# Optimization experiments

Measured on AMD Instinct MI355X. Metric: run time of the kernel, lower is better.

## Reference

```python
import jax, jax.numpy as jnp
import numpy as np

B, S, D = 4, 512, 2048      # batch, seq, hidden
DFF = 5632                   # SwiGLU intermediate
E, TOPK, R = 8, 2, 16        # experts, top-k, lora rank
SCALE = 32.0 / 16.0          # lora alpha / r


def setup_inputs() -> dict:
    key = jax.random.key(0)
    ks = jax.random.split(key, 18)
    rn = lambda k, shape, s=0.02: (jax.random.normal(k, shape, dtype=jnp.float32) * s)
    return {
        "data": jax.random.normal(ks[0], (B, S, D), dtype=jnp.float32),
        # shared base SwiGLU MLP (gate/up/down projections)
        "W1": rn(ks[1], (DFF, D)),
        "W3": rn(ks[2], (DFF, D)),
        "W2": rn(ks[3], (D, DFF)),
        # MixLoRA MoE adapter: router gate + per-expert LoRA on w1/w3/w2
        "gate_W": rn(ks[4], (E, D)),
        "A1": rn(ks[5], (E, R, D)), "B1": rn(ks[6], (E, DFF, R)),
        "A3": rn(ks[7], (E, R, D)), "B3": rn(ks[8], (E, DFF, R)),
        "A2": rn(ks[9], (E, R, DFF)), "B2": rn(ks[10], (E, D, R)),
        # plain LoRA adapter (second batch segment, _lora_forward path)
        "la1": rn(ks[11], (R, D)), "lb1": rn(ks[12], (DFF, R)),
        "la3": rn(ks[13], (R, D)), "lb3": rn(ks[14], (DFF, R)),
        "la2": rn(ks[15], (R, DFF)), "lb2": rn(ks[16], (D, R)),
    }


def reference(data, W1, W3, W2, gate_W, A1, B1, A3, B3, A2, B2,
              la1, lb1, la3, lb3, la2, lb2):
    half = B // 2

    # ---- segment 0: MixLoRA MoE adapter ----
    x = data[:half].reshape(-1, D)                      # [N, D] tokens
    N = x.shape[0]
    logits = x @ gate_W.T                               # [N, E] router logits
    probs = jax.nn.softmax(logits, axis=-1)
    topw, topi = jax.lax.top_k(probs, TOPK)
    topw = topw / jnp.sum(topw, axis=-1, keepdims=True)
    # dense routing weights (zero for non-selected experts)
    wd = jnp.zeros((N, E), x.dtype).at[jnp.arange(N)[:, None], topi].set(topw)

    bg = x @ W1.T                                       # [N, DFF] base gate proj
    bu = x @ W3.T                                       # [N, DFF] base up proj
    dg = jnp.einsum('enr,efr->enf', jnp.einsum('nd,erd->enr', x, A1), B1)
    du = jnp.einsum('enr,efr->enf', jnp.einsum('nd,erd->enr', x, A3), B3)
    h = jax.nn.silu(bg[None] + SCALE * dg) * (bu[None] + SCALE * du)  # [E,N,DFF]
    oe = jnp.einsum('enf,df->end', h, W2) \
        + SCALE * jnp.einsum('enr,edr->end', jnp.einsum('enf,erf->enr', h, A2), B2)
    moe_out = jnp.einsum('ne,end->nd', wd, oe).reshape(half, S, D)

    # ---- segment 1: plain LoRA adapter (_lora_forward) ----
    x2 = data[half:]                                    # [half, S, D]
    g2 = jax.nn.silu(x2 @ W1.T + SCALE * ((x2 @ la1.T) @ lb1.T))
    u2 = x2 @ W3.T + SCALE * ((x2 @ la3.T) @ lb3.T)
    h2 = g2 * u2
    out2 = h2 @ W2.T + SCALE * ((h2 @ la2.T) @ lb2.T)

    # index_copy over contiguous per-segment ranges == concat along dim 0
    final = jnp.concatenate([moe_out, out2], axis=0)    # [B, S, D]
    return final, logits
```

## Files before the change

### kernel.cpp

```cpp
#include <hip/hip_runtime.h>
#include <hip/hip_bf16.h>

#define DEVI __device__ __forceinline__

typedef __attribute__((ext_vector_type(8))) short short8;
typedef __attribute__((ext_vector_type(4))) float f32x4;

constexpr int D    = 2048;
constexpr int DFF  = 5632;
constexpr int NTOK = 2048;
constexpr int NMOE = 1024;
constexpr float KSCALE = 2.0f;

constexpr int NW      = 11776;
constexpr int COL_A1  = 11264;
constexpr int COL_A3  = 11392;
constexpr int COL_LA1 = 11520;
constexpr int COL_LA3 = 11536;

DEVI float bf2f(unsigned short u) { return __uint_as_float(((unsigned)u) << 16); }
DEVI unsigned short f2bf(float f) {
  unsigned u = __float_as_uint(f);
  u += 0x7FFFu + ((u >> 16) & 1u);
  return (unsigned short)(u >> 16);
}
DEVI float silu(float x) { return x / (1.f + __expf(-x)); }

struct CastSegs {
  const float* src[14];
  unsigned short* dst[14];
  int blk_end[14];
};

__global__ __launch_bounds__(256) void cast_segs_kernel(CastSegs cs) {
  int b = blockIdx.x;
  int s = 0;
  #pragma unroll
  for (int i = 0; i < 14; ++i) if (b >= cs.blk_end[i]) s = i + 1;
  int bstart = (s == 0) ? 0 : cs.blk_end[s - 1];
  size_t idx = ((size_t)(b - bstart) * 256 + threadIdx.x) * 4;
  float4 v = *(const float4*)(cs.src[s] + idx);
  ushort4 o;
  o.x = f2bf(v.x); o.y = f2bf(v.y); o.z = f2bf(v.z); o.w = f2bf(v.w);
  *(ushort4*)(cs.dst[s] + idx) = o;
}

__global__ __launch_bounds__(256) void transpose_ra_kernel(const float* __restrict__ A2,
                                                           const float* __restrict__ la2,
                                                           unsigned short* __restrict__ A2tb,
                                                           unsigned short* __restrict__ la2tb) {
  int f = blockIdx.x * 256 + threadIdx.x;
  int e = blockIdx.y;
  const float* src = (e < 8) ? (A2 + (size_t)e * 16 * DFF) : la2;
  unsigned short* dst = (e < 8) ? (A2tb + (size_t)e * DFF * 16) : la2tb;
  unsigned short tmp[16];
  #pragma unroll
  for (int r = 0; r < 16; ++r) tmp[r] = f2bf(src[(size_t)r * DFF + f]);
  #pragma unroll
  for (int r = 0; r < 16; ++r) dst[(size_t)f * 16 + r] = tmp[r];
}

__global__ __launch_bounds__(256) void gate_kernel(const float* __restrict__ x,
                                                   const float* __restrict__ gW,
                                                   float* __restrict__ logits_out,
                                                   int* __restrict__ gidx,
                                                   float* __restrict__ gwt) {
  int t = blockIdx.x * 4 + (threadIdx.x >> 6);
  int lane = threadIdx.x & 63;
  const float* xr = x + (size_t)t * D;
  float acc[8];
  #pragma unroll
  for (int e = 0; e < 8; ++e) acc[e] = 0.f;
  for (int k = lane; k < D; k += 64) {
    float xv = xr[k];
    #pragma unroll
    for (int e = 0; e < 8; ++e) acc[e] = fmaf(xv, gW[e * D + k], acc[e]);
  }
  #pragma unroll
  for (int e = 0; e < 8; ++e) {
    float v = acc[e];
    #pragma unroll
    for (int s = 32; s > 0; s >>= 1) v += __shfl_xor(v, s);
    acc[e] = v;
  }
  if (lane == 0) {
    #pragma unroll
    for (int e = 0; e < 8; ++e) logits_out[(size_t)t * 8 + e] = acc[e];
    int i1 = 0;
    #pragma unroll
    for (int e = 1; e < 8; ++e) if (acc[e] > acc[i1]) i1 = e;
    int i2 = (i1 == 0) ? 1 : 0;
    #pragma unroll
    for (int e = 0; e < 8; ++e) if (e != i1 && acc[e] > acc[i2]) i2 = e;
    float w1 = 1.f / (1.f + expf(acc[i2] - acc[i1]));
    gidx[t * 2] = i1; gidx[t * 2 + 1] = i2;
    gwt[t * 2] = w1;  gwt[t * 2 + 1] = 1.f - w1;
  }
}

typedef const void __attribute__((address_space(1)))* gp1_t;
typedef void __attribute__((address_space(3)))* lp3_t;
DEVI void gload_lds16(const void* g, void* l) {
  __builtin_amdgcn_global_load_lds((gp1_t)g, (lp3_t)l, 16, 0, 0);
}
#define S_BARRIER() asm volatile("s_barrier" ::: "memory")

template <int N> DEVI void vmcnt_() {
  static_assert(N == 0 || N == 4 || N == 6 || N == 8 || N == 12, "enumerate literals");
  if constexpr (N == 0)  asm volatile("s_waitcnt vmcnt(0)" ::: "memory");
  if constexpr (N == 4)  asm volatile("s_waitcnt vmcnt(4)" ::: "memory");
  if constexpr (N == 6)  asm volatile("s_waitcnt vmcnt(6)" ::: "memory");
  if constexpr (N == 8)  asm volatile("s_waitcnt vmcnt(8)" ::: "memory");
  if constexpr (N == 12) asm volatile("s_waitcnt vmcnt(12)" ::: "memory");
}

template <int BM, int BN, int WM, int WN, int NBUF, int NPH, int MINW, int EPI>
__global__ __launch_bounds__(WM * WN * 64, MINW) void gemmT(
    const unsigned short* __restrict__ A,
    const unsigned short* __restrict__ B,
    int K,
    float* __restrict__ Cf,
    unsigned short* __restrict__ Cb,
    const float* __restrict__ addv,
    int ldc, int nbx) {
  constexpr int THREADS = WM * WN * 64;
  constexpr int RW = BM / WM;
  constexpr int CW = BN / WN;
  constexpr int FM = RW / 16, FN = CW / 16;
  constexpr int FMP = FM / NPH;
  constexpr int ATILE = BM * 128;
  constexpr int BTILE = BN * 128;
  constexpr int SLOT = ATILE + BTILE;
  constexpr int APARTS = BM * 8 / THREADS;
  constexpr int BPARTS = BN * 8 / THREADS;
  constexpr int LOADS = APARTS + BPARTS;
  constexpr int PD = NBUF - 1;

  __shared__ __align__(16) char smem[NBUF * SLOT];

  const int tid = threadIdx.x;
  const int wave = tid >> 6, lane = tid & 63;
  const int wm = wave / WN, wn = wave % WN;
  const int r15 = lane & 15, g = lane >> 4;

  const int nwg = (int)gridDim.x;
  const int bid = (int)blockIdx.x;
  const int wgid = (bid & 7) * (nwg >> 3) + (bid >> 3);
  const int bx = wgid % nbx, by = wgid / nbx;

  const unsigned short* Ablk = A + (size_t)by * BM * K;
  const unsigned short* Bblk = B + (size_t)bx * BN * K;

  int sgoA[APARTS], sgoB[BPARTS];
  #pragma unroll
  for (int j = 0; j < APARTS; ++j) {
    int tt = j * THREADS + tid;
    int row = tt >> 3;
    sgoA[j] = row * K + (((tt & 7) ^ (row & 7)) << 3);
  }
  #pragma unroll
  for (int j = 0; j < BPARTS; ++j) {
    int tt = j * THREADS + tid;
    int row = tt >> 3;
    sgoB[j] = row * K + (((tt & 7) ^ (row & 7)) << 3);
  }
  auto stage = [&](int slot, int k0) {
    char* s = smem + slot * SLOT;
    #pragma unroll
    for (int j = 0; j < APARTS; ++j)
      gload_lds16((const char*)Ablk + ((size_t)(sgoA[j] + k0) << 1),
                  s + j * (THREADS * 16) + wave * 1024);
    #pragma unroll
    for (int j = 0; j < BPARTS; ++j)
      gload_lds16((const char*)Bblk + ((size_t)(sgoB[j] + k0) << 1),
                  s + ATILE + j * (THREADS * 16) + wave * 1024);
  };

  const int arow0 = (wm * RW + r15) * 128;
  const int brow0 = (wn * CW + r15) * 128;
  const int s0 = ((g ^ (r15 & 7)) << 4);
  const int s1 = (((4 + g) ^ (r15 & 7)) << 4);

  f32x4 acc[FM][FN];
  #pragma unroll
  for (int m = 0; m < FM; ++m)
    #pragma unroll
    for (int n = 0; n < FN; ++n)
      #pragma unroll
      for (int j = 0; j < 4; ++j) acc[m][n][j] = 0.f;

  const int NT = K >> 6;

  #pragma unroll
  for (int d = 0; d < PD; ++d) stage(d, d << 6);

  int slCur = 0, slAhead = PD % NBUF;
  for (int t = 0; t < NT; ++t) {
    if (t + PD < NT) {
      stage(slAhead, (t + PD) << 6);
      vmcnt_<PD * LOADS>();
    } else if (PD == 2 && t + 1 < NT) {
      vmcnt_<LOADS>();
    } else {
      vmcnt_<0>();
    }
    S_BARRIER();

    const char* sA = smem + slCur * SLOT;
    const char* sB = sA + ATILE;
    short8 bq[FN][2];
    #pragma unroll
    for (int n = 0; n < FN; ++n) {
      bq[n][0] = *(const short8*)(sB + brow0 + n * 16 * 128 + s0);
      bq[n][1] = *(const short8*)(sB + brow0 + n * 16 * 128 + s1);
    }
    #pragma unroll
    for (int p = 0; p < NPH; ++p) {
      short8 af[FMP][2];
      #pragma unroll
      for (int i = 0; i < FMP; ++i) {
        int ro = arow0 + (p * FMP + i) * 16 * 128;
        af[i][0] = *(const short8*)(sA + ro + s0);
        af[i][1] = *(const short8*)(sA + ro + s1);
      }
      __builtin_amdgcn_s_setprio(1);
      #pragma unroll
      for (int i = 0; i < FMP; ++i)
        #pragma unroll
        for (int n = 0; n < FN; ++n)
          #pragma unroll
          for (int kk = 0; kk < 2; ++kk)
            acc[p * FMP + i][n] = __builtin_amdgcn_mfma_f32_16x16x32_bf16(
                af[i][kk], bq[n][kk], acc[p * FMP + i][n], 0, 0, 0);
      __builtin_amdgcn_s_setprio(0);
    }
    S_BARRIER();
    slCur = (slCur + 1 == NBUF) ? 0 : slCur + 1;
    slAhead = (slAhead + 1 == NBUF) ? 0 : slAhead + 1;
  }

  const int row0 = by * BM + wm * RW + (g << 2);
  const int col0 = bx * BN + wn * CW + r15;
  #pragma unroll
  for (int m = 0; m < FM; ++m) {
    #pragma unroll
    for (int n = 0; n < FN; ++n) {
      int col = col0 + n * 16;
      #pragma unroll
      for (int j = 0; j < 4; ++j) {
        int row = row0 + m * 16 + j;
        size_t off = (size_t)row * ldc + col;
        float v = acc[m][n][j];
        if (EPI == 1) Cb[off] = f2bf(v);
        else          Cf[off] = v + addv[off];
      }
    }
  }
}

DEVI float dot16bf(const float* a, const unsigned short* w) {
  short8 w0 = *(const short8*)w;
  short8 w1 = *(const short8*)(w + 8);
  float s = 0.f;
  #pragma unroll
  for (int i = 0; i < 8; ++i) s = fmaf(a[i],     bf2f((unsigned short)w0[i]), s);
  #pragma unroll
  for (int i = 0; i < 8; ++i) s = fmaf(a[8 + i], bf2f((unsigned short)w1[i]), s);
  return s;
}

__global__ __launch_bounds__(256) void h_kernel(
    const unsigned short* __restrict__ GU,
    const unsigned short* __restrict__ B1b,
    const unsigned short* __restrict__ B3b,
    const unsigned short* __restrict__ A2tb,
    const unsigned short* __restrict__ lb1b,
    const unsigned short* __restrict__ lb3b,
    const unsigned short* __restrict__ la2tb,
    const int* __restrict__ gidx, const float* __restrict__ gwt,
    unsigned short* __restrict__ Hb,
    float* __restrict__ qw) {
  const int t = blockIdx.x;
  const int tid = threadIdx.x;
  const unsigned short* gu = GU + (size_t)t * NW;
  unsigned short* hrow = Hb + (size_t)t * DFF;
  float qacc[32];
  #pragma unroll
  for (int r = 0; r < 32; ++r) qacc[r] = 0.f;
  float w1 = 0.f, w2 = 0.f;

  if (t < NMOE) {
    const int e1 = gidx[t * 2], e2 = gidx[t * 2 + 1];
    w1 = gwt[t * 2]; w2 = gwt[t * 2 + 1];
    float xa1a[16], xa1b[16], xa3a[16], xa3b[16];
    #pragma unroll
    for (int r = 0; r < 16; ++r) {
      xa1a[r] = bf2f(gu[COL_A1 + e1 * 16 + r]);
      xa1b[r] = bf2f(gu[COL_A1 + e2 * 16 + r]);
      xa3a[r] = bf2f(gu[COL_A3 + e1 * 16 + r]);
      xa3b[r] = bf2f(gu[COL_A3 + e2 * 16 + r]);
    }
    const unsigned short* B1e1 = B1b + (size_t)e1 * DFF * 16;
    const unsigned short* B1e2 = B1b + (size_t)e2 * DFF * 16;
    const unsigned short* B3e1 = B3b + (size_t)e1 * DFF * 16;
    const unsigned short* B3e2 = B3b + (size_t)e2 * DFF * 16;
    const unsigned short* A2e1 = A2tb + (size_t)e1 * DFF * 16;
    const unsigned short* A2e2 = A2tb + (size_t)e2 * DFF * 16;
    for (int i = 0; i < 22; ++i) {
      int f = tid + i * 256;
      float bg = bf2f(gu[f]), bu = bf2f(gu[DFF + f]);
      float dg1 = dot16bf(xa1a, B1e1 + f * 16);
      float du1 = dot16bf(xa3a, B3e1 + f * 16);
      float dg2 = dot16bf(xa1b, B1e2 + f * 16);
      float du2 = dot16bf(xa3b, B3e2 + f * 16);
      float h1 = silu(bg + KSCALE * dg1) * (bu + KSCALE * du1);
      float h2 = silu(bg + KSCALE * dg2) * (bu + KSCALE * du2);
      hrow[f] = f2bf(w1 * h1 + w2 * h2);
      short8 a0 = *(const short8*)(A2e1 + f * 16);
      short8 a1 = *(const short8*)(A2e1 + f * 16 + 8);
      short8 b0 = *(const short8*)(A2e2 + f * 16);
      short8 b1 = *(const short8*)(A2e2 + f * 16 + 8);
      #pragma unroll
      for (int r = 0; r < 8; ++r) {
        qacc[r]      = fmaf(h1, bf2f((unsigned short)a0[r]), qacc[r]);
        qacc[8 + r]  = fmaf(h1, bf2f((unsigned short)a1[r]), qacc[8 + r]);
        qacc[16 + r] = fmaf(h2, bf2f((unsigned short)b0[r]), qacc[16 + r]);
        qacc[24 + r] = fmaf(h2, bf2f((unsigned short)b1[r]), qacc[24 + r]);
      }
    }
  } else {
    float s1[16], s3[16];
    #pragma unroll
    for (int r = 0; r < 16; ++r) {
      s1[r] = bf2f(gu[COL_LA1 + r]);
      s3[r] = bf2f(gu[COL_LA3 + r]);
    }
    for (int i = 0; i < 22; ++i) {
      int f = tid + i * 256;
      float bg = bf2f(gu[f]), bu = bf2f(gu[DFF + f]);
      float dg = dot16bf(s1, lb1b + f * 16);
      float du = dot16bf(s3, lb3b + f * 16);
      float h = silu(bg + KSCALE * dg) * (bu + KSCALE * du);
      hrow[f] = f2bf(h);
      short8 a0 = *(const short8*)(la2tb + f * 16);
      short8 a1 = *(const short8*)(la2tb + f * 16 + 8);
      #pragma unroll
      for (int r = 0; r < 8; ++r) {
        qacc[r]     = fmaf(h, bf2f((unsigned short)a0[r]), qacc[r]);
        qacc[8 + r] = fmaf(h, bf2f((unsigned short)a1[r]), qacc[8 + r]);
      }
    }
  }

  #pragma unroll
  for (int r = 0; r < 32; ++r) {
    float v = qacc[r];
    #pragma unroll
    for (int s = 32; s > 0; s >>= 1) v += __shfl_xor(v, s);
    qacc[r] = v;
  }
  __shared__ float red[4][32];
  const int wave = tid >> 6, lane = tid & 63;
  if (lane == 0) {
    #pragma unroll
    for (int r = 0; r < 32; ++r) red[wave][r] = qacc[r];
  }
  __syncthreads();
  if (tid < 32) {
    float v = red[0][tid] + red[1][tid] + red[2][tid] + red[3][tid];
    float sc = (t < NMOE) ? ((tid < 16) ? (KSCALE * w1) : (KSCALE * w2)) : KSCALE;
    qw[(size_t)t * 32 + tid] = v * sc;
  }
}

__global__ __launch_bounds__(256) void ylora_kernel(const float* __restrict__ qw,
                                                    const unsigned short* __restrict__ B2b,
                                                    const unsigned short* __restrict__ lb2b,
                                                    const int* __restrict__ gidx,
                                                    float* __restrict__ ylora) {
  const int t = blockIdx.x;
  const int tid = threadIdx.x;
  const float* qr = qw + (size_t)t * 32;
  float q1[16], q2[16];
  #pragma unroll
  for (int r = 0; r < 16; ++r) { q1[r] = qr[r]; q2[r] = qr[16 + r]; }
  if (t < NMOE) {
    const unsigned short* p1 = B2b + (size_t)gidx[t * 2] * D * 16;
    const unsigned short* p2 = B2b + (size_t)gidx[t * 2 + 1] * D * 16;
    #pragma unroll
    for (int i = 0; i < 8; ++i) {
      int d = tid + i * 256;
      ylora[(size_t)t * D + d] = dot16bf(q1, p1 + d * 16) + dot16bf(q2, p2 + d * 16);
    }
  } else {
    #pragma unroll
    for (int i = 0; i < 8; ++i) {
      int d = tid + i * 256;
      ylora[(size_t)t * D + d] = dot16bf(q1, lb2b + d * 16);
    }
  }
}

extern "C" void kernel_launch(void* const* d_in, const int* in_sizes, int n_in,
                              void* d_out, int out_size, void* d_ws, size_t ws_size,
                              hipStream_t stream) {
  (void)in_sizes; (void)n_in; (void)out_size; (void)ws_size;
  const float* data = (const float*)d_in[0];
  const float* W1   = (const float*)d_in[1];
  const float* W3   = (const float*)d_in[2];
  const float* W2   = (const float*)d_in[3];
  const float* gW   = (const float*)d_in[4];
  const float* A1   = (const float*)d_in[5];
  const float* B1   = (const float*)d_in[6];
  const float* A3   = (const float*)d_in[7];
  const float* B3   = (const float*)d_in[8];
  const float* A2   = (const float*)d_in[9];
  const float* B2   = (const float*)d_in[10];
  const float* la1  = (const float*)d_in[11];
  const float* lb1  = (const float*)d_in[12];
  const float* la3  = (const float*)d_in[13];
  const float* lb3  = (const float*)d_in[14];
  const float* la2  = (const float*)d_in[15];
  const float* lb2  = (const float*)d_in[16];

  char* w = (char*)d_ws;
  size_t off = 0;
  auto alloc = [&](size_t bytes) -> char* {
    char* p = w + off;
    off += (bytes + 255) & ~(size_t)255;
    return p;
  };
  unsigned short* xb    = (unsigned short*)alloc((size_t)NTOK * D * 2);
  unsigned short* W13b  = (unsigned short*)alloc((size_t)NW * D * 2);
  unsigned short* W2b   = (unsigned short*)alloc((size_t)D * DFF * 2);
  unsigned short* B1b   = (unsigned short*)alloc((size_t)8 * DFF * 16 * 2);
  unsigned short* B3b   = (unsigned short*)alloc((size_t)8 * DFF * 16 * 2);
  unsigned short* A2tb  = (unsigned short*)alloc((size_t)8 * DFF * 16 * 2);
  unsigned short* la2tb = (unsigned short*)alloc((size_t)DFF * 16 * 2);
  unsigned short* lb1b  = (unsigned short*)alloc((size_t)DFF * 16 * 2);
  unsigned short* lb3b  = (unsigned short*)alloc((size_t)DFF * 16 * 2);
  unsigned short* lb2b  = (unsigned short*)alloc((size_t)D * 16 * 2);
  unsigned short* B2b   = (unsigned short*)alloc((size_t)8 * D * 16 * 2);
  int*   gidx = (int*)alloc((size_t)NMOE * 2 * 4);
  float* gwt  = (float*)alloc((size_t)NMOE * 2 * 4);
  unsigned short* GU    = (unsigned short*)alloc((size_t)NTOK * NW * 2);

  unsigned short* Hb = W13b;
  float* ylora = (float*)((char*)W13b + (size_t)NTOK * DFF * 2);
  float* qw    = (float*)xb;

  CastSegs cs;
  const float* srcs[14] = {data, W1, W3, W2, A1, A3, la1, la3, B1, B3, lb1, lb3, lb2, B2};
  unsigned short* dsts[14] = {
      xb, W13b, W13b + (size_t)DFF * D, W2b,
      W13b + (size_t)COL_A1 * D, W13b + (size_t)COL_A3 * D,
      W13b + (size_t)COL_LA1 * D, W13b + (size_t)COL_LA3 * D,
      B1b, B3b, lb1b, lb3b, lb2b, B2b};
  int ns[14] = {NTOK * D, DFF * D, DFF * D, DFF * D, 128 * D, 128 * D, 16 * D, 16 * D,
                8 * DFF * 16, 8 * DFF * 16, DFF * 16, DFF * 16, D * 16, 8 * D * 16};
  int total_blocks = 0;
  for (int i = 0; i < 14; ++i) {
    cs.src[i] = srcs[i];
    cs.dst[i] = dsts[i];
    total_blocks += ns[i] / 1024;
    cs.blk_end[i] = total_blocks;
  }
  cast_segs_kernel<<<total_blocks, 256, 0, stream>>>(cs);
  transpose_ra_kernel<<<dim3(DFF / 256, 9), 256, 0, stream>>>(A2, la2, A2tb, la2tb);
  hipMemsetAsync(W13b + (size_t)11552 * D, 0, (size_t)(NW - 11552) * D * 2, stream);

  gate_kernel<<<NMOE / 4, 256, 0, stream>>>(data, gW,
      (float*)d_out + (size_t)NTOK * D, gidx, gwt);

  gemmT<256, 256, 2, 4, 2, 4, 2, 1><<<(NTOK / 256) * (NW / 256), 512, 0, stream>>>(
      xb, W13b, D, (float*)nullptr, GU, (const float*)nullptr, NW, NW / 256);

  h_kernel<<<NTOK, 256, 0, stream>>>(GU, B1b, B3b, A2tb, lb1b, lb3b, la2tb,
                                     gidx, gwt, Hb, qw);

  ylora_kernel<<<NTOK, 256, 0, stream>>>(qw, B2b, lb2b, gidx, ylora);

  gemmT<128, 128, 2, 4, 3, 2, 4, 2><<<(NTOK / 128) * (D / 128), 512, 0, stream>>>(
      Hb, W2b, DFF, (float*)d_out, (unsigned short*)nullptr, ylora, D, D / 128);
}
```

Measured before the change: 363.1 us.

## Replace multi-buffer GEMM pipeline with double-buffered ping-pong schedule with barriers

Replaces the templated NBUF/NPH GEMM with a fixed two-buffer kernel that splits each K-tile into two halves of A fragments. Each half gets an extra workgroup barrier and an explicit LDS wait before its MFMA burst, in a ping-pong style meant to interleave waves' memory and compute phases. The down-projection GEMM drops from three buffers to two, which cuts LDS and may raise occupancy. The cost is shallower prefetch depth and more barriers per iteration.

```diff
diff --git a/kernel.cpp b/kernel.cpp
--- a/kernel.cpp
+++ b/kernel.cpp
@@ -104,18 +104,18 @@
   __builtin_amdgcn_global_load_lds((gp1_t)g, (lp3_t)l, 16, 0, 0);
 }
 #define S_BARRIER() asm volatile("s_barrier" ::: "memory")
+#define LGKM0() do { asm volatile("s_waitcnt lgkmcnt(0)" ::: "memory"); \
+                     __builtin_amdgcn_sched_barrier(0); } while (0)
 
 template <int N> DEVI void vmcnt_() {
-  static_assert(N == 0 || N == 4 || N == 6 || N == 8 || N == 12, "enumerate literals");
+  static_assert(N == 0 || N == 4 || N == 8, "enumerate literals");
   if constexpr (N == 0)  asm volatile("s_waitcnt vmcnt(0)" ::: "memory");
   if constexpr (N == 4)  asm volatile("s_waitcnt vmcnt(4)" ::: "memory");
-  if constexpr (N == 6)  asm volatile("s_waitcnt vmcnt(6)" ::: "memory");
   if constexpr (N == 8)  asm volatile("s_waitcnt vmcnt(8)" ::: "memory");
-  if constexpr (N == 12) asm volatile("s_waitcnt vmcnt(12)" ::: "memory");
-}
-
-template <int BM, int BN, int WM, int WN, int NBUF, int NPH, int MINW, int EPI>
-__global__ __launch_bounds__(WM * WN * 64, MINW) void gemmT(
+}
+
+template <int BM, int BN, int WM, int WN, int MINW, int EPI>
+__global__ __launch_bounds__(WM * WN * 64, MINW) void gemm8p(
     const unsigned short* __restrict__ A,
     const unsigned short* __restrict__ B,
     int K,
@@ -127,16 +127,15 @@
   constexpr int RW = BM / WM;
   constexpr int CW = BN / WN;
   constexpr int FM = RW / 16, FN = CW / 16;
-  constexpr int FMP = FM / NPH;
+  constexpr int FM2 = FM / 2;
   constexpr int ATILE = BM * 128;
   constexpr int BTILE = BN * 128;
   constexpr int SLOT = ATILE + BTILE;
   constexpr int APARTS = BM * 8 / THREADS;
   constexpr int BPARTS = BN * 8 / THREADS;
   constexpr int LOADS = APARTS + BPARTS;
-  constexpr int PD = NBUF - 1;
-
-  __shared__ __align__(16) char smem[NBUF * SLOT];
+
+  __shared__ __align__(16) char smem[2 * SLOT];
 
   const int tid = threadIdx.x;
   const int wave = tid >> 6, lane = tid & 63;
@@ -191,52 +190,68 @@
 
   const int NT = K >> 6;
 
-  #pragma unroll
-  for (int d = 0; d < PD; ++d) stage(d, d << 6);
-
-  int slCur = 0, slAhead = PD % NBUF;
+  stage(0, 0);
+
   for (int t = 0; t < NT; ++t) {
-    if (t + PD < NT) {
-      stage(slAhead, (t + PD) << 6);
-      vmcnt_<PD * LOADS>();
-    } else if (PD == 2 && t + 1 < NT) {
+    const int cur = t & 1;
+    if (t + 1 < NT) {
+      stage(cur ^ 1, (t + 1) << 6);
       vmcnt_<LOADS>();
     } else {
       vmcnt_<0>();
     }
     S_BARRIER();
 
-    const char* sA = smem + slCur * SLOT;
+    const char* sA = smem + cur * SLOT;
     const char* sB = sA + ATILE;
+
     short8 bq[FN][2];
     #pragma unroll
     for (int n = 0; n < FN; ++n) {
       bq[n][0] = *(const short8*)(sB + brow0 + n * 16 * 128 + s0);
       bq[n][1] = *(const short8*)(sB + brow0 + n * 16 * 128 + s1);
     }
-    #pragma unroll
-    for (int p = 0; p < NPH; ++p) {
-      short8 af[FMP][2];
+    short8 af0[FM2][2];
+    #pragma unroll
+    for (int i = 0; i < FM2; ++i) {
+      int ro = arow0 + i * 16 * 128;
+      af0[i][0] = *(const short8*)(sA + ro + s0);
+      af0[i][1] = *(const short8*)(sA + ro + s1);
+    }
+    S_BARRIER();
+    LGKM0();
+    __builtin_amdgcn_s_setprio(1);
+    #pragma unroll
+    for (int i = 0; i < FM2; ++i)
       #pragma unroll
-      for (int i = 0; i < FMP; ++i) {
-        int ro = arow0 + (p * FMP + i) * 16 * 128;
-        af[i][0] = *(const short8*)(sA + ro + s0);
-        af[i][1] = *(const short8*)(sA + ro + s1);
-      }
-      __builtin_amdgcn_s_setprio(1);
+      for (int n = 0; n < FN; ++n)
+        #pragma unroll
+        for (int kk = 0; kk < 2; ++kk)
+          acc[i][n] = __builtin_amdgcn_mfma_f32_16x16x32_bf16(
+              af0[i][kk], bq[n][kk], acc[i][n], 0, 0, 0);
+    __builtin_amdgcn_s_setprio(0);
+
+    short8 af1[FM2][2];
+    #pragma unroll
+    for (int i = 0; i < FM2; ++i) {
+      int ro = arow0 + (FM2 + i) * 16 * 128;
+      af1[i][0] = *(const short8*)(sA + ro + s0);
+      af1[i][1] = *(const short8*)(sA + ro + s1);
+    }
+    S_BARRIER();
+    LGKM0();
+    __builtin_amdgcn_s_setprio(1);
+    #pragma unroll
+    for (int i = 0; i < FM2; ++i)
       #pragma unroll
-      for (int i = 0; i < FMP; ++i)
+      for (int n = 0; n < FN; ++n)
         #pragma unroll
-        for (int n = 0; n < FN; ++n)
-          #pragma unroll
-          for (int kk = 0; kk < 2; ++kk)
-            acc[p * FMP + i][n] = __builtin_amdgcn_mfma_f32_16x16x32_bf16(
-                af[i][kk], bq[n][kk], acc[p * FMP + i][n], 0, 0, 0);
-      __builtin_amdgcn_s_setprio(0);
-    }
+        for (int kk = 0; kk < 2; ++kk)
+          acc[FM2 + i][n] = __builtin_amdgcn_mfma_f32_16x16x32_bf16(
+              af1[i][kk], bq[n][kk], acc[FM2 + i][n], 0, 0, 0);
+    __builtin_amdgcn_s_setprio(0);
+
     S_BARRIER();
-    slCur = (slCur + 1 == NBUF) ? 0 : slCur + 1;
-    slAhead = (slAhead + 1 == NBUF) ? 0 : slAhead + 1;
   }
 
   const int row0 = by * BM + wm * RW + (g << 2);
@@ -472,7 +487,7 @@
   gate_kernel<<<NMOE / 4, 256, 0, stream>>>(data, gW,
       (float*)d_out + (size_t)NTOK * D, gidx, gwt);
 
-  gemmT<256, 256, 2, 4, 2, 4, 2, 1><<<(NTOK / 256) * (NW / 256), 512, 0, stream>>>(
+  gemm8p<256, 256, 2, 4, 2, 1><<<(NTOK / 256) * (NW / 256), 512, 0, stream>>>(
       xb, W13b, D, (float*)nullptr, GU, (const float*)nullptr, NW, NW / 256);
 
   h_kernel<<<NTOK, 256, 0, stream>>>(GU, B1b, B3b, A2tb, lb1b, lb3b, la2tb,
@@ -480,6 +495,6 @@
 
   ylora_kernel<<<NTOK, 256, 0, stream>>>(qw, B2b, lb2b, gidx, ylora);
 
-  gemmT<128, 128, 2, 4, 3, 2, 4, 2><<<(NTOK / 128) * (D / 128), 512, 0, stream>>>(
+  gemm8p<128, 128, 2, 4, 4, 2><<<(NTOK / 128) * (D / 128), 512, 0, stream>>>(
       Hb, W2b, DFF, (float*)d_out, (unsigned short*)nullptr, ylora, D, D / 128);
 }
```

Measured after the change: 367.1 us. Within noise of the previous version (+1.1%).
